# Performance work log

Hardware: AMD Instinct MI355X
Metric: run time of the kernel (lower is better)

The kernel has to match this reference:

```python
import jax, jax.numpy as jnp
import numpy as np

V_TGT, V_CMP = 100, 100
E_ENC, E_DEC = 5, 128
H_ENC, H_DEC = 256, 512
B, S, T = 128, 120, 120
GO = 0


def _p(key, shape, scale=0.08):
    return scale * jax.random.normal(key, shape, dtype=jnp.float32)


def setup_inputs() -> dict:
    key = jax.random.key(0)
    ks = iter(jax.random.split(key, 48))
    inp = {}
    inp['tgts'] = jax.random.randint(next(ks), (B, S), 0, V_TGT)
    inp['cmps'] = jax.random.randint(next(ks), (B, T), 0, V_CMP)
    inp['emb_enc'] = _p(next(ks), (V_TGT, E_ENC))
    for d in ('f', 'b'):
        inp['enc_Wih_' + d] = _p(next(ks), (3 * H_ENC, E_ENC))
        inp['enc_Whh_' + d] = _p(next(ks), (3 * H_ENC, H_ENC))
        inp['enc_bih_' + d] = jnp.zeros((3 * H_ENC,), jnp.float32)
        inp['enc_bhh_' + d] = jnp.zeros((3 * H_ENC,), jnp.float32)
    inp['emb_dec'] = _p(next(ks), (V_CMP, E_DEC))
    inp['attn_W'] = _p(next(ks), (H_DEC, 2 * H_DEC))
    inp['attn_b'] = jnp.zeros((H_DEC,), jnp.float32)
    inp['attn_v'] = _p(next(ks), (H_DEC,))
    dims = [E_DEC + H_DEC, H_DEC, H_DEC]
    for l in range(3):
        inp['dec_Wih%d' % l] = _p(next(ks), (3 * H_DEC, dims[l]))
        inp['dec_Whh%d' % l] = _p(next(ks), (3 * H_DEC, H_DEC))
        inp['dec_bih%d' % l] = jnp.zeros((3 * H_DEC,), jnp.float32)
        inp['dec_bhh%d' % l] = jnp.zeros((3 * H_DEC,), jnp.float32)
    inp['out_W'] = _p(next(ks), (V_CMP, H_DEC))
    inp['out_b'] = jnp.zeros((V_CMP,), jnp.float32)
    return inp


def gru_cell(x, h, Wih, Whh, bih, bhh):
    gi = x @ Wih.T + bih
    gh = h @ Whh.T + bhh
    ir, iz, inn = jnp.split(gi, 3, axis=-1)
    hr, hz, hn = jnp.split(gh, 3, axis=-1)
    r = jax.nn.sigmoid(ir + hr)
    z = jax.nn.sigmoid(iz + hz)
    n = jnp.tanh(inn + r * hn)
    return (1.0 - z) * n + z * h


def run_gru(xs, h0, Wih, Whh, bih, bhh, reverse=False):
    # xs: (S, B, in); returns outputs (S, B, H) and final hidden (B, H)
    def step(h, x):
        h2 = gru_cell(x, h, Wih, Whh, bih, bhh)
        return h2, h2
    hT, outs = jax.lax.scan(step, h0, xs, reverse=reverse)
    return outs, hT


def _forward(tgts, cmps, emb_enc, enc_Wih_f, enc_Whh_f, enc_bih_f, enc_bhh_f,
             enc_Wih_b, enc_Whh_b, enc_bih_b, enc_bhh_b, emb_dec,
             attn_W, attn_b, attn_v,
             dec_Wih0, dec_Whh0, dec_bih0, dec_bhh0,
             dec_Wih1, dec_Whh1, dec_bih1, dec_bhh1,
             dec_Wih2, dec_Whh2, dec_bih2, dec_bhh2,
             out_W, out_b):
    b = tgts.shape[0]
    # ---- encoder: bidirectional GRU ----
    xs = emb_enc[tgts].transpose(1, 0, 2)  # (S, B, E_ENC)
    h0 = jnp.zeros((b, H_ENC), jnp.float32)
    out_f, h_f = run_gru(xs, h0, enc_Wih_f, enc_Whh_f, enc_bih_f, enc_bhh_f)
    out_b_, h_b = run_gru(xs, h0, enc_Wih_b, enc_Whh_b, enc_bih_b, enc_bhh_b, reverse=True)
    enc_out = jnp.concatenate([out_f, out_b_], -1).transpose(1, 0, 2)  # (B, S, 512)
    h_enc = jnp.concatenate([h_f, h_b], -1)                             # (B, 512)
    hidden = jnp.zeros((3, b, H_DEC), jnp.float32).at[0].set(h_enc)
    # ---- decoder: teacher-forced inputs [GO, cmps[:, :-1]] ----
    x_seq = jnp.concatenate([jnp.full((b, 1), GO, cmps.dtype), cmps[:, :-1]], 1).T  # (T, B)

    def dec_step(h, x_t):
        emb = emb_dec[x_t]                                   # (B, 128)
        hq = h[0]                                            # (B, 512)
        cat = jnp.concatenate(
            [jnp.broadcast_to(hq[:, None, :], enc_out.shape), enc_out], -1)  # (B, S, 1024)
        energy = jnp.tanh(cat @ attn_W.T + attn_b)           # (B, S, 512)
        score = energy @ attn_v                              # (B, S)
        attn = jax.nn.softmax(score, axis=-1)
        ctx = jnp.einsum('bs,bsh->bh', attn, enc_out)        # (B, 512)
        inp = jnp.concatenate([emb, ctx], -1)                # (B, 640)
        h0n = gru_cell(inp, h[0], dec_Wih0, dec_Whh0, dec_bih0, dec_bhh0)
        h1n = gru_cell(h0n, h[1], dec_Wih1, dec_Whh1, dec_bih1, dec_bhh1)
        h2n = gru_cell(h1n, h[2], dec_Wih2, dec_Whh2, dec_bih2, dec_bhh2)
        logit = h2n @ out_W.T + out_b                        # (B, V_CMP)
        return jnp.stack([h0n, h1n, h2n]), jax.nn.log_softmax(logit, axis=-1)

    _, scores = jax.lax.scan(jax.checkpoint(dec_step), hidden, x_seq)
    return scores.transpose(1, 0, 2)  # (B, T, V_CMP)


def reference(tgts, cmps, emb_enc, enc_Wih_f, enc_Whh_f, enc_bih_f, enc_bhh_f,
              enc_Wih_b, enc_Whh_b, enc_bih_b, enc_bhh_b, emb_dec,
              attn_W, attn_b, attn_v,
              dec_Wih0, dec_Whh0, dec_bih0, dec_bhh0,
              dec_Wih1, dec_Whh1, dec_bih1, dec_bhh1,
              dec_Wih2, dec_Whh2, dec_bih2, dec_bhh2,
              out_W, out_b):
    return _forward(tgts, cmps, emb_enc, enc_Wih_f, enc_Whh_f, enc_bih_f, enc_bhh_f,
                    enc_Wih_b, enc_Whh_b, enc_bih_b, enc_bhh_b, emb_dec,
                    attn_W, attn_b, attn_v,
                    dec_Wih0, dec_Whh0, dec_bih0, dec_bhh0,
                    dec_Wih1, dec_Whh1, dec_bih1, dec_bhh1,
                    dec_Wih2, dec_Whh2, dec_bih2, dec_bhh2,
                    out_W, out_b)
```

## Files before the change

### kernel.cpp

```cpp
#include <hip/hip_runtime.h>
#include <math.h>

#define B_   128
#define S_   120
#define T_   120
#define HENC 256
#define HDEC 512
#define VCMP 100

#define OFF_EMBGI_F   0
#define OFF_EMBGI_B   76800
#define OFF_EMBGI_D   153600
#define OFF_HENC      307200
#define OFF_HDEC      438272
#define OFF_HQP       831488
#define OFF_CTX       1093632
#define OFF_GIP       1159168
#define OFF_GHP       1945600
#define OFF_ENCOUT    2732032
#define OFF_ENCATT    10596352
#define WS_FLOATS     18460672

#define PSTRIDE_D 196608
#define PSTRIDE_Q 65536

__device__ __forceinline__ float sigm(float x)      { return 1.0f / (1.0f + __expf(-x)); }
__device__ __forceinline__ float tanh_fast(float x) { return 1.0f - 2.0f / (1.0f + __expf(2.0f * x)); }

__device__ __forceinline__ float wred_sum(float v) {
#pragma unroll
  for (int m = 32; m > 0; m >>= 1) v += __shfl_xor(v, m);
  return v;
}
__device__ __forceinline__ float wred_max(float v) {
#pragma unroll
  for (int m = 32; m > 0; m >>= 1) v = fmaxf(v, __shfl_xor(v, m));
  return v;
}

__global__ void k_zero(float* p, int n) {
  int i = blockIdx.x * blockDim.x + threadIdx.x;
  if (i < n) p[i] = 0.0f;
}

__global__ void k_embgi_enc(const float* emb, const float* Wf, const float* bf,
                            const float* Wb, const float* bb, float* outf, float* outb) {
  int idx = blockIdx.x * blockDim.x + threadIdx.x;
  const float* W  = blockIdx.y ? Wb : Wf;
  const float* bi = blockIdx.y ? bb : bf;
  float* o        = blockIdx.y ? outb : outf;
  int v = idx / 768, j = idx % 768;
  float a = bi[j];
#pragma unroll
  for (int e = 0; e < 5; e++) a = fmaf(emb[v * 5 + e], W[j * 5 + e], a);
  o[idx] = a;
}

__global__ void k_embgi_dec(const float* emb, const float* Wih0, const float* bih0, float* out) {
  int idx = blockIdx.x * blockDim.x + threadIdx.x;
  int v = idx / 1536, j = idx % 1536;
  float a = bih0[j];
  const float4* er = (const float4*)(emb + v * 128);
  const float4* wr = (const float4*)(Wih0 + (size_t)j * 640);
#pragma unroll 8
  for (int e = 0; e < 32; e++) {
    float4 ev = er[e], wv = wr[e];
    a = fmaf(ev.x, wv.x, a); a = fmaf(ev.y, wv.y, a);
    a = fmaf(ev.z, wv.z, a); a = fmaf(ev.w, wv.w, a);
  }
  out[idx] = a;
}

struct GemmJob {
  const float* A; const float* W; float* C; const float* bias;
  int lda, ldw, N;
};

__global__ __launch_bounds__(256) void k_gemm64(GemmJob ja, GemmJob jb, int splits, int Kc, int Cstride) {
  GemmJob jj = ((int)blockIdx.z < splits) ? ja : jb;
  int sp = blockIdx.z % splits;
  int k0 = sp * Kc;
  float* C = jj.C + (size_t)sp * Cstride;
  int tid = threadIdx.x;
  int tx = tid & 15, ty = tid >> 4;
  int m0 = blockIdx.y * 64, n0 = blockIdx.x * 64;
  __shared__ float As[16][68];
  __shared__ float Ws[16][68];
  float acc[4][4] = {};
  int r = tid >> 2, c = tid & 3;
  const float* Ap = jj.A + (size_t)(m0 + r) * jj.lda + k0 + c * 4;
  const float* Wp = jj.W + (size_t)(n0 + r) * jj.ldw + k0 + c * 4;
  for (int kt = 0; kt < Kc; kt += 16) {
    float4 av = *(const float4*)(Ap + kt);
    float4 wv = *(const float4*)(Wp + kt);
    __syncthreads();
    As[c * 4 + 0][r] = av.x; As[c * 4 + 1][r] = av.y; As[c * 4 + 2][r] = av.z; As[c * 4 + 3][r] = av.w;
    Ws[c * 4 + 0][r] = wv.x; Ws[c * 4 + 1][r] = wv.y; Ws[c * 4 + 2][r] = wv.z; Ws[c * 4 + 3][r] = wv.w;
    __syncthreads();
#pragma unroll
    for (int kk = 0; kk < 16; kk++) {
      float4 a = *(const float4*)&As[kk][ty * 4];
      float4 w = *(const float4*)&Ws[kk][tx * 4];
      float am[4] = {a.x, a.y, a.z, a.w}, wn[4] = {w.x, w.y, w.z, w.w};
#pragma unroll
      for (int i = 0; i < 4; i++)
#pragma unroll
        for (int j2 = 0; j2 < 4; j2++) acc[i][j2] = fmaf(am[i], wn[j2], acc[i][j2]);
    }
  }
  int N = jj.N;
  float bv[4] = {0, 0, 0, 0};
  if (jj.bias) {
#pragma unroll
    for (int j2 = 0; j2 < 4; j2++) bv[j2] = jj.bias[n0 + tx * 4 + j2];
  }
#pragma unroll
  for (int i = 0; i < 4; i++) {
    float4 v = {acc[i][0] + bv[0], acc[i][1] + bv[1], acc[i][2] + bv[2], acc[i][3] + bv[3]};
    *(float4*)(C + (size_t)(m0 + ty * 4 + i) * N + n0 + tx * 4) = v;
  }
}

__global__ __launch_bounds__(256) void k_gemm128(GemmJob ja, GemmJob jb, int splits, int Kc, int Cstride) {
  GemmJob jj = ((int)blockIdx.z < splits) ? ja : jb;
  int sp = blockIdx.z % splits;
  int k0 = sp * Kc;
  float* C = jj.C + (size_t)sp * Cstride;
  int tid = threadIdx.x;
  int tx = tid & 15, ty = tid >> 4;
  int m0 = blockIdx.y * 128, n0 = blockIdx.x * 128;
  __shared__ float As[16][132];
  __shared__ float Ws[16][132];
  float acc[8][8] = {};
  for (int kt = 0; kt < Kc; kt += 16) {
    float4 av[2], wv[2];
#pragma unroll
    for (int h = 0; h < 2; h++) {
      int idx = tid + h * 256;
      int r = idx >> 2, c = idx & 3;
      av[h] = *(const float4*)(jj.A + (size_t)(m0 + r) * jj.lda + k0 + kt + c * 4);
      wv[h] = *(const float4*)(jj.W + (size_t)(n0 + r) * jj.ldw + k0 + kt + c * 4);
    }
    __syncthreads();
#pragma unroll
    for (int h = 0; h < 2; h++) {
      int idx = tid + h * 256;
      int r = idx >> 2, c = idx & 3;
      As[c * 4 + 0][r] = av[h].x; As[c * 4 + 1][r] = av[h].y; As[c * 4 + 2][r] = av[h].z; As[c * 4 + 3][r] = av[h].w;
      Ws[c * 4 + 0][r] = wv[h].x; Ws[c * 4 + 1][r] = wv[h].y; Ws[c * 4 + 2][r] = wv[h].z; Ws[c * 4 + 3][r] = wv[h].w;
    }
    __syncthreads();
#pragma unroll
    for (int kk = 0; kk < 16; kk++) {
      float4 a0 = *(const float4*)&As[kk][ty * 4];
      float4 a1 = *(const float4*)&As[kk][ty * 4 + 64];
      float4 w0 = *(const float4*)&Ws[kk][tx * 4];
      float4 w1 = *(const float4*)&Ws[kk][tx * 4 + 64];
      float am[8] = {a0.x, a0.y, a0.z, a0.w, a1.x, a1.y, a1.z, a1.w};
      float wn[8] = {w0.x, w0.y, w0.z, w0.w, w1.x, w1.y, w1.z, w1.w};
#pragma unroll
      for (int i = 0; i < 8; i++)
#pragma unroll
        for (int j2 = 0; j2 < 8; j2++) acc[i][j2] = fmaf(am[i], wn[j2], acc[i][j2]);
    }
  }
  int N = jj.N;
  float bv[8] = {0, 0, 0, 0, 0, 0, 0, 0};
  if (jj.bias) {
#pragma unroll
    for (int j2 = 0; j2 < 4; j2++) {
      bv[j2]     = jj.bias[n0 + tx * 4 + j2];
      bv[4 + j2] = jj.bias[n0 + 64 + tx * 4 + j2];
    }
  }
#pragma unroll
  for (int i = 0; i < 8; i++) {
    int m = m0 + ((i < 4) ? (ty * 4 + i) : (64 + ty * 4 + (i - 4)));
    float4 v0 = {acc[i][0] + bv[0], acc[i][1] + bv[1], acc[i][2] + bv[2], acc[i][3] + bv[3]};
    float4 v1 = {acc[i][4] + bv[4], acc[i][5] + bv[5], acc[i][6] + bv[6], acc[i][7] + bv[7]};
    *(float4*)(C + (size_t)m * N + n0 + tx * 4) = v0;
    *(float4*)(C + (size_t)m * N + n0 + 64 + tx * 4) = v1;
  }
}

__global__ void k_gate_enc(const float* ghP, const float* tabf, const float* tabb,
                           const float* bhhf, const float* bhhb, const int* tgts,
                           const float* hfc, float* hfn, const float* hbc, float* hbn,
                           float* enc_out, int t) {
  int g = blockIdx.x * blockDim.x + threadIdx.x;
  int d = g >> 15, rem = g & 32767, b = rem >> 8, j = rem & 255;
  int sidx = d ? (S_ - 1 - t) : t;
  int tok = tgts[b * S_ + sidx];
  const float* gh  = ghP + (size_t)(d * 2) * PSTRIDE_D + b * 768;
  const float* bh  = d ? bhhb : bhhf;
  const float* tab = (d ? tabb : tabf) + (size_t)tok * 768;
  float hr  = gh[j]       + gh[PSTRIDE_D + j]       + bh[j];
  float hz  = gh[j + 256] + gh[PSTRIDE_D + j + 256] + bh[j + 256];
  float hnn = gh[j + 512] + gh[PSTRIDE_D + j + 512] + bh[j + 512];
  float rr = sigm(tab[j] + hr);
  float zz = sigm(tab[j + 256] + hz);
  float nn = tanh_fast(tab[j + 512] + rr * hnn);
  const float* hc = d ? hbc : hfc;
  float*       hx = d ? hbn : hfn;
  float h0 = hc[b * 256 + j];
  float h2 = (1.0f - zz) * nn + zz * h0;
  hx[b * 256 + j] = h2;
  enc_out[((size_t)b * S_ + sidx) * 512 + d * 256 + j] = h2;
}

__global__ void k_h0init(const float* hf, const float* hb, float* h0) {
  int g = blockIdx.x * blockDim.x + threadIdx.x;
  int b = g >> 9, j = g & 511;
  h0[g] = (j < 256) ? hf[b * 256 + j] : hb[b * 256 + (j - 256)];
}

__global__ __launch_bounds__(256) void k_att_ctx(const float* hqP, const float* enc_att,
                                                 const float* enc_out, const float* av,
                                                 float* ctx) {
  int b = blockIdx.x;
  __shared__ float hq[512];
  __shared__ float vs[512];
  __shared__ float sc[128];
  __shared__ float red[8];
  int tid = threadIdx.x, w = tid >> 6, lane = tid & 63;
  for (int d = tid; d < 512; d += 256) {
    hq[d] = hqP[b * 512 + d] + hqP[PSTRIDE_Q + b * 512 + d] +
            hqP[2 * PSTRIDE_Q + b * 512 + d] + hqP[3 * PSTRIDE_Q + b * 512 + d];
    vs[d] = av[d];
  }
  __syncthreads();
  for (int i = 0; i < 30; i++) {
    int s = w + 4 * i;
    const float4* ea = (const float4*)(enc_att + ((size_t)b * S_ + s) * 512) + lane * 2;
    float4 e0 = ea[0], e1 = ea[1];
    int d0 = lane * 8;
    float a;
    a  = vs[d0 + 0] * tanh_fast(e0.x + hq[d0 + 0]);
    a += vs[d0 + 1] * tanh_fast(e0.y + hq[d0 + 1]);
    a += vs[d0 + 2] * tanh_fast(e0.z + hq[d0 + 2]);
    a += vs[d0 + 3] * tanh_fast(e0.w + hq[d0 + 3]);
    a += vs[d0 + 4] * tanh_fast(e1.x + hq[d0 + 4]);
    a += vs[d0 + 5] * tanh_fast(e1.y + hq[d0 + 5]);
    a += vs[d0 + 6] * tanh_fast(e1.z + hq[d0 + 6]);
    a += vs[d0 + 7] * tanh_fast(e1.w + hq[d0 + 7]);
    a = wred_sum(a);
    if (lane == 0) sc[s] = a;
  }
  __syncthreads();
  float x = (tid < S_) ? sc[tid] : -1e30f;
  float mx = wred_max(x);
  if (lane == 0) red[w] = mx;
  __syncthreads();
  mx = fmaxf(fmaxf(red[0], red[1]), fmaxf(red[2], red[3]));
  float e = (tid < S_) ? __expf(x - mx) : 0.0f;
  float sm = wred_sum(e);
  if (lane == 0) red[4 + w] = sm;
  __syncthreads();
  float inv = 1.0f / (red[4] + red[5] + red[6] + red[7]);
  if (tid < S_) sc[tid] = e * inv;
  __syncthreads();
  for (int h = tid; h < 512; h += 256) {
    float cacc = 0.0f;
    const float* eo = enc_out + (size_t)b * S_ * 512 + h;
#pragma unroll 4
    for (int s = 0; s < S_; s++) cacc = fmaf(sc[s], eo[(size_t)s * 512], cacc);
    ctx[b * 512 + h] = cacc;
  }
}

__global__ void k_gate_dec(const float* giP, const float* ghP, const float* gtab,
                           const int* cmps, int t, const float* bih, const float* bhh,
                           const float* hp, float* hn) {
  int g = blockIdx.x * blockDim.x + threadIdx.x;
  int b = g >> 9, j = g & 511;
  int base = b * 1536 + j;
  float gr  = giP[base]        + giP[PSTRIDE_D + base]        + giP[2 * PSTRIDE_D + base]        + giP[3 * PSTRIDE_D + base];
  float gz  = giP[base + 512]  + giP[PSTRIDE_D + base + 512]  + giP[2 * PSTRIDE_D + base + 512]  + giP[3 * PSTRIDE_D + base + 512];
  float gn  = giP[base + 1024] + giP[PSTRIDE_D + base + 1024] + giP[2 * PSTRIDE_D + base + 1024] + giP[3 * PSTRIDE_D + base + 1024];
  float hr  = ghP[base]        + ghP[PSTRIDE_D + base]        + ghP[2 * PSTRIDE_D + base]        + ghP[3 * PSTRIDE_D + base]        + bhh[j];
  float hz  = ghP[base + 512]  + ghP[PSTRIDE_D + base + 512]  + ghP[2 * PSTRIDE_D + base + 512]  + ghP[3 * PSTRIDE_D + base + 512]  + bhh[j + 512];
  float hnn = ghP[base + 1024] + ghP[PSTRIDE_D + base + 1024] + ghP[2 * PSTRIDE_D + base + 1024] + ghP[3 * PSTRIDE_D + base + 1024] + bhh[j + 1024];
  float er, ez, en;
  if (gtab) {
    int tok = (t == 0) ? 0 : cmps[b * T_ + (t - 1)];
    const float* row = gtab + (size_t)tok * 1536;
    er = row[j]; ez = row[j + 512]; en = row[j + 1024];
  } else {
    er = bih[j]; ez = bih[j + 512]; en = bih[j + 1024];
  }
  float rr = sigm(gr + er + hr);
  float zz = sigm(gz + ez + hz);
  float nn = tanh_fast(gn + en + rr * hnn);
  float h0 = hp[b * 512 + j];
  hn[b * 512 + j] = (1.0f - zz) * nn + zz * h0;
}

__global__ __launch_bounds__(256) void k_out(const float* h2, const float* oW, const float* ob,
                                             float* out, int t) {
  int b = blockIdx.x;
  __shared__ float hs[512];
  __shared__ float lg[104];
  __shared__ float red[8];
  int tid = threadIdx.x, w = tid >> 6, lane = tid & 63;
  for (int d = tid; d < 512; d += 256) hs[d] = h2[b * 512 + d];
  __syncthreads();
  for (int i = 0; i < 25; i++) {
    int n = w + 4 * i;
    const float4* wr = (const float4*)(oW + (size_t)n * 512) + lane * 2;
    float4 w0 = wr[0], w1 = wr[1];
    const float* hp = &hs[lane * 8];
    float a = w0.x * hp[0] + w0.y * hp[1] + w0.z * hp[2] + w0.w * hp[3] +
              w1.x * hp[4] + w1.y * hp[5] + w1.z * hp[6] + w1.w * hp[7];
    a = wred_sum(a);
    if (lane == 0) lg[n] = a + ob[n];
  }
  __syncthreads();
  float x = (tid < VCMP) ? lg[tid] : -1e30f;
  float mx = wred_max(x);
  if (lane == 0) red[w] = mx;
  __syncthreads();
  mx = fmaxf(fmaxf(red[0], red[1]), fmaxf(red[2], red[3]));
  float e = (tid < VCMP) ? __expf(x - mx) : 0.0f;
  float sm = wred_sum(e);
  if (lane == 0) red[4 + w] = sm;
  __syncthreads();
  float lse = mx + logf(red[4] + red[5] + red[6] + red[7]);
  if (tid < VCMP) out[((size_t)b * T_ + t) * VCMP + tid] = x - lse;
}

extern "C" void kernel_launch(void* const* d_in, const int* in_sizes, int n_in,
                              void* d_out, int out_size, void* d_ws, size_t ws_size,
                              hipStream_t stream) {
  (void)in_sizes; (void)n_in; (void)out_size; (void)ws_size;
  const int*   tgts    = (const int*)d_in[0];
  const int*   cmps    = (const int*)d_in[1];
  const float* emb_enc = (const float*)d_in[2];
  const float* eWih_f  = (const float*)d_in[3];
  const float* eWhh_f  = (const float*)d_in[4];
  const float* ebih_f  = (const float*)d_in[5];
  const float* ebhh_f  = (const float*)d_in[6];
  const float* eWih_b  = (const float*)d_in[7];
  const float* eWhh_b  = (const float*)d_in[8];
  const float* ebih_b  = (const float*)d_in[9];
  const float* ebhh_b  = (const float*)d_in[10];
  const float* emb_dec = (const float*)d_in[11];
  const float* attn_W  = (const float*)d_in[12];
  const float* attn_b  = (const float*)d_in[13];
  const float* attn_v  = (const float*)d_in[14];
  const float* dWih0   = (const float*)d_in[15];
  const float* dWhh0   = (const float*)d_in[16];
  const float* dbih0   = (const float*)d_in[17];  (void)dbih0;
  const float* dbhh0   = (const float*)d_in[18];
  const float* dWih1   = (const float*)d_in[19];
  const float* dWhh1   = (const float*)d_in[20];
  const float* dbih1   = (const float*)d_in[21];
  const float* dbhh1   = (const float*)d_in[22];
  const float* dWih2   = (const float*)d_in[23];
  const float* dWhh2   = (const float*)d_in[24];
  const float* dbih2   = (const float*)d_in[25];
  const float* dbhh2   = (const float*)d_in[26];
  const float* out_W   = (const float*)d_in[27];
  const float* out_b   = (const float*)d_in[28];
  float* out = (float*)d_out;
  float* ws  = (float*)d_ws;

  float* emb_gi_f = ws + OFF_EMBGI_F;
  float* emb_gi_b = ws + OFF_EMBGI_B;
  float* emb_gi_d = ws + OFF_EMBGI_D;
  float* h_enc    = ws + OFF_HENC;
  float* h_dec    = ws + OFF_HDEC;
  float* hqP      = ws + OFF_HQP;
  float* ctx      = ws + OFF_CTX;
  float* giP      = ws + OFF_GIP;
  float* ghP      = ws + OFF_GHP;
  float* enc_out  = ws + OFF_ENCOUT;
  float* enc_att  = ws + OFF_ENCATT;

  k_embgi_enc<<<dim3(300, 2), 256, 0, stream>>>(emb_enc, eWih_f, ebih_f, eWih_b, ebih_b, emb_gi_f, emb_gi_b);
  k_embgi_dec<<<600, 256, 0, stream>>>(emb_dec, dWih0, dbih0, emb_gi_d);
  {
    int nz = 2 * 2 * B_ * HENC + 2 * 3 * B_ * HDEC;
    k_zero<<<(nz + 255) / 256, 256, 0, stream>>>(h_enc, nz);
  }

  for (int t = 0; t < S_; t++) {
    int cur = t & 1, nxt = cur ^ 1;
    GemmJob ja = {h_enc + 0 * 65536 + cur * 32768, eWhh_f, giP, nullptr, 256, 256, 768};
    GemmJob jb = {h_enc + 1 * 65536 + cur * 32768, eWhh_b, giP + 2 * PSTRIDE_D, nullptr, 256, 256, 768};
    k_gemm64<<<dim3(12, 2, 4), 256, 0, stream>>>(ja, jb, 2, 128, PSTRIDE_D);
    k_gate_enc<<<256, 256, 0, stream>>>(giP, emb_gi_f, emb_gi_b, ebhh_f, ebhh_b, tgts,
                                        h_enc + cur * 32768, h_enc + nxt * 32768,
                                        h_enc + 65536 + cur * 32768, h_enc + 65536 + nxt * 32768,
                                        enc_out, t);
  }
  k_h0init<<<256, 256, 0, stream>>>(h_enc, h_enc + 65536, h_dec);

  {
    GemmJob ja = {enc_out, attn_W + 512, enc_att, attn_b, 512, 1024, 512};
    k_gemm128<<<dim3(4, 120, 1), 256, 0, stream>>>(ja, ja, 1, 512, 0);
  }

  for (int t = 0; t < T_; t++) {
    int cur = t & 1, nxt = cur ^ 1;
    float* h0c = h_dec + cur * 196608;
    float* h1c = h0c + 65536;
    float* h2c = h0c + 131072;
    float* h0n = h_dec + nxt * 196608;
    float* h1n = h0n + 65536;
    float* h2n = h0n + 131072;
    (void)h2c;

    GemmJob jq = {h0c, attn_W, hqP, nullptr, 512, 1024, 512};
    k_gemm64<<<dim3(8, 2, 4), 256, 0, stream>>>(jq, jq, 4, 128, PSTRIDE_Q);
    k_att_ctx<<<128, 256, 0, stream>>>(hqP, enc_att, enc_out, attn_v, ctx);

    GemmJob g0a = {ctx, dWih0 + 128, giP, nullptr, 512, 640, 1536};
    GemmJob g0b = {h0c, dWhh0, ghP, nullptr, 512, 512, 1536};
    k_gemm128<<<dim3(12, 1, 8), 256, 0, stream>>>(g0a, g0b, 4, 128, PSTRIDE_D);
    k_gate_dec<<<256, 256, 0, stream>>>(giP, ghP, emb_gi_d, cmps, t, nullptr, dbhh0, h0c, h0n);

    GemmJob g1a = {h0n, dWih1, giP, nullptr, 512, 512, 1536};
    GemmJob g1b = {h1c, dWhh1, ghP, nullptr, 512, 512, 1536};
    k_gemm128<<<dim3(12, 1, 8), 256, 0, stream>>>(g1a, g1b, 4, 128, PSTRIDE_D);
    k_gate_dec<<<256, 256, 0, stream>>>(giP, ghP, nullptr, nullptr, t, dbih1, dbhh1, h1c, h1n);

    GemmJob g2a = {h1n, dWih2, giP, nullptr, 512, 512, 1536};
    GemmJob g2b = {h2c, dWhh2, ghP, nullptr, 512, 512, 1536};
    k_gemm128<<<dim3(12, 1, 8), 256, 0, stream>>>(g2a, g2b, 4, 128, PSTRIDE_D);
    k_gate_dec<<<256, 256, 0, stream>>>(giP, ghP, nullptr, nullptr, t, dbih2, dbhh2, h2c, h2n);

    k_out<<<128, 256, 0, stream>>>(h2n, out_W, out_b, out, t);
  }
}
```

Before: 17.35 ms.

## Rewrite encoder/decoder recurrences with fp16 MFMA fused GEMM+gate kernels

Replaces the fp32 SIMT GEMMs with fp16 MFMA 16x16x32 kernels and fuses each GRU step's hidden GEMM with its gate nonlinearity. All recurrent-weight matmuls that depend only on the previous step's hidden states (attention query plus the three decoder Whh) are batched into one concatenated-weight GEMM per step. The output projection and log-softmax are moved out of the time loop into one batched GEMM over all steps. Weights, encoder outputs and attention keys are converted to fp16 up front, cutting launch count and memory traffic, at the cost of reduced precision in the recurrent path.

```diff
diff --git a/kernel.cpp b/kernel.cpp
--- a/kernel.cpp
+++ b/kernel.cpp
@@ -4,25 +4,36 @@
 #define B_   128
 #define S_   120
 #define T_   120
-#define HENC 256
-#define HDEC 512
 #define VCMP 100
 
-#define OFF_EMBGI_F   0
-#define OFF_EMBGI_B   76800
-#define OFF_EMBGI_D   153600
-#define OFF_HENC      307200
-#define OFF_HDEC      438272
-#define OFF_HQP       831488
-#define OFF_CTX       1093632
-#define OFF_GIP       1159168
-#define OFF_GHP       1945600
-#define OFF_ENCOUT    2732032
-#define OFF_ENCATT    10596352
-#define WS_FLOATS     18460672
-
-#define PSTRIDE_D 196608
-#define PSTRIDE_Q 65536
+typedef _Float16 f16;
+typedef _Float16 f16x8 __attribute__((ext_vector_type(8)));
+typedef float f32x4 __attribute__((ext_vector_type(4)));
+
+#define MFMA16(a,b,c) __builtin_amdgcn_mfma_f32_16x16x32_f16(a, b, c, 0, 0, 0)
+
+#define OFF_TAB_F    0
+#define OFF_TAB_B    76800
+#define OFF_TAB_D    153600
+#define OFF_HENC32   307200
+#define OFF_HENC16   438272
+#define OFF_HDEC32   503808
+#define OFF_HDEC16   897024
+#define OFF_CA       1028096
+#define OFF_CTX32    1683456
+#define OFF_CTX16    1748992
+#define OFF_H2ALL    1781760
+#define OFF_ENCOUT   5746688
+#define OFF_ENCATT   9678848
+#define OFF_LOGITS   13611008
+#define OFF_WCAT     15577088
+#define OFF_WIH0C    16887808
+#define OFF_WIH1     17281024
+#define OFF_WIH2     17674240
+#define OFF_UE       18067456
+#define OFF_EWHH     18198528
+#define OFF_OW       18395136
+#define WS_FLOATS    18427904
 
 __device__ __forceinline__ float sigm(float x)      { return 1.0f / (1.0f + __expf(-x)); }
 __device__ __forceinline__ float tanh_fast(float x) { return 1.0f - 2.0f / (1.0f + __expf(2.0f * x)); }
@@ -41,6 +52,13 @@
 __global__ void k_zero(float* p, int n) {
   int i = blockIdx.x * blockDim.x + threadIdx.x;
   if (i < n) p[i] = 0.0f;
+}
+
+__global__ void k_cvt(const float* src, f16* dst, int rows, int cols, int ldsrc, int off) {
+  int i = blockIdx.x * blockDim.x + threadIdx.x;
+  if (i >= rows * cols) return;
+  int r = i / cols, c = i - r * cols;
+  dst[(size_t)r * cols + c] = (f16)src[(size_t)r * ldsrc + off + c];
 }
 
 __global__ void k_embgi_enc(const float* emb, const float* Wf, const float* bf,
@@ -71,152 +89,166 @@
   out[idx] = a;
 }
 
-struct GemmJob {
-  const float* A; const float* W; float* C; const float* bias;
-  int lda, ldw, N;
-};
-
-__global__ __launch_bounds__(256) void k_gemm64(GemmJob ja, GemmJob jb, int splits, int Kc, int Cstride) {
-  GemmJob jj = ((int)blockIdx.z < splits) ? ja : jb;
-  int sp = blockIdx.z % splits;
-  int k0 = sp * Kc;
-  float* C = jj.C + (size_t)sp * Cstride;
-  int tid = threadIdx.x;
-  int tx = tid & 15, ty = tid >> 4;
-  int m0 = blockIdx.y * 64, n0 = blockIdx.x * 64;
-  __shared__ float As[16][68];
-  __shared__ float Ws[16][68];
-  float acc[4][4] = {};
-  int r = tid >> 2, c = tid & 3;
-  const float* Ap = jj.A + (size_t)(m0 + r) * jj.lda + k0 + c * 4;
-  const float* Wp = jj.W + (size_t)(n0 + r) * jj.ldw + k0 + c * 4;
-  for (int kt = 0; kt < Kc; kt += 16) {
-    float4 av = *(const float4*)(Ap + kt);
-    float4 wv = *(const float4*)(Wp + kt);
-    __syncthreads();
-    As[c * 4 + 0][r] = av.x; As[c * 4 + 1][r] = av.y; As[c * 4 + 2][r] = av.z; As[c * 4 + 3][r] = av.w;
-    Ws[c * 4 + 0][r] = wv.x; Ws[c * 4 + 1][r] = wv.y; Ws[c * 4 + 2][r] = wv.z; Ws[c * 4 + 3][r] = wv.w;
-    __syncthreads();
-#pragma unroll
-    for (int kk = 0; kk < 16; kk++) {
-      float4 a = *(const float4*)&As[kk][ty * 4];
-      float4 w = *(const float4*)&Ws[kk][tx * 4];
-      float am[4] = {a.x, a.y, a.z, a.w}, wn[4] = {w.x, w.y, w.z, w.w};
-#pragma unroll
-      for (int i = 0; i < 4; i++)
-#pragma unroll
-        for (int j2 = 0; j2 < 4; j2++) acc[i][j2] = fmaf(am[i], wn[j2], acc[i][j2]);
-    }
-  }
-  int N = jj.N;
-  float bv[4] = {0, 0, 0, 0};
-  if (jj.bias) {
-#pragma unroll
-    for (int j2 = 0; j2 < 4; j2++) bv[j2] = jj.bias[n0 + tx * 4 + j2];
-  }
-#pragma unroll
-  for (int i = 0; i < 4; i++) {
-    float4 v = {acc[i][0] + bv[0], acc[i][1] + bv[1], acc[i][2] + bv[2], acc[i][3] + bv[3]};
-    *(float4*)(C + (size_t)(m0 + ty * 4 + i) * N + n0 + tx * 4) = v;
-  }
-}
-
-__global__ __launch_bounds__(256) void k_gemm128(GemmJob ja, GemmJob jb, int splits, int Kc, int Cstride) {
-  GemmJob jj = ((int)blockIdx.z < splits) ? ja : jb;
-  int sp = blockIdx.z % splits;
-  int k0 = sp * Kc;
-  float* C = jj.C + (size_t)sp * Cstride;
-  int tid = threadIdx.x;
-  int tx = tid & 15, ty = tid >> 4;
-  int m0 = blockIdx.y * 128, n0 = blockIdx.x * 128;
-  __shared__ float As[16][132];
-  __shared__ float Ws[16][132];
-  float acc[8][8] = {};
-  for (int kt = 0; kt < Kc; kt += 16) {
-    float4 av[2], wv[2];
-#pragma unroll
-    for (int h = 0; h < 2; h++) {
-      int idx = tid + h * 256;
-      int r = idx >> 2, c = idx & 3;
-      av[h] = *(const float4*)(jj.A + (size_t)(m0 + r) * jj.lda + k0 + kt + c * 4);
-      wv[h] = *(const float4*)(jj.W + (size_t)(n0 + r) * jj.ldw + k0 + kt + c * 4);
-    }
-    __syncthreads();
-#pragma unroll
-    for (int h = 0; h < 2; h++) {
-      int idx = tid + h * 256;
-      int r = idx >> 2, c = idx & 3;
-      As[c * 4 + 0][r] = av[h].x; As[c * 4 + 1][r] = av[h].y; As[c * 4 + 2][r] = av[h].z; As[c * 4 + 3][r] = av[h].w;
-      Ws[c * 4 + 0][r] = wv[h].x; Ws[c * 4 + 1][r] = wv[h].y; Ws[c * 4 + 2][r] = wv[h].z; Ws[c * 4 + 3][r] = wv[h].w;
-    }
-    __syncthreads();
-#pragma unroll
-    for (int kk = 0; kk < 16; kk++) {
-      float4 a0 = *(const float4*)&As[kk][ty * 4];
-      float4 a1 = *(const float4*)&As[kk][ty * 4 + 64];
-      float4 w0 = *(const float4*)&Ws[kk][tx * 4];
-      float4 w1 = *(const float4*)&Ws[kk][tx * 4 + 64];
-      float am[8] = {a0.x, a0.y, a0.z, a0.w, a1.x, a1.y, a1.z, a1.w};
-      float wn[8] = {w0.x, w0.y, w0.z, w0.w, w1.x, w1.y, w1.z, w1.w};
-#pragma unroll
-      for (int i = 0; i < 8; i++)
-#pragma unroll
-        for (int j2 = 0; j2 < 8; j2++) acc[i][j2] = fmaf(am[i], wn[j2], acc[i][j2]);
-    }
-  }
-  int N = jj.N;
-  float bv[8] = {0, 0, 0, 0, 0, 0, 0, 0};
-  if (jj.bias) {
-#pragma unroll
-    for (int j2 = 0; j2 < 4; j2++) {
-      bv[j2]     = jj.bias[n0 + tx * 4 + j2];
-      bv[4 + j2] = jj.bias[n0 + 64 + tx * 4 + j2];
-    }
-  }
-#pragma unroll
-  for (int i = 0; i < 8; i++) {
-    int m = m0 + ((i < 4) ? (ty * 4 + i) : (64 + ty * 4 + (i - 4)));
-    float4 v0 = {acc[i][0] + bv[0], acc[i][1] + bv[1], acc[i][2] + bv[2], acc[i][3] + bv[3]};
-    float4 v1 = {acc[i][4] + bv[4], acc[i][5] + bv[5], acc[i][6] + bv[6], acc[i][7] + bv[7]};
-    *(float4*)(C + (size_t)m * N + n0 + tx * 4) = v0;
-    *(float4*)(C + (size_t)m * N + n0 + 64 + tx * 4) = v1;
-  }
-}
-
-__global__ void k_gate_enc(const float* ghP, const float* tabf, const float* tabb,
-                           const float* bhhf, const float* bhhb, const int* tgts,
-                           const float* hfc, float* hfn, const float* hbc, float* hbn,
-                           float* enc_out, int t) {
-  int g = blockIdx.x * blockDim.x + threadIdx.x;
-  int d = g >> 15, rem = g & 32767, b = rem >> 8, j = rem & 255;
-  int sidx = d ? (S_ - 1 - t) : t;
-  int tok = tgts[b * S_ + sidx];
-  const float* gh  = ghP + (size_t)(d * 2) * PSTRIDE_D + b * 768;
-  const float* bh  = d ? bhhb : bhhf;
-  const float* tab = (d ? tabb : tabf) + (size_t)tok * 768;
-  float hr  = gh[j]       + gh[PSTRIDE_D + j]       + bh[j];
-  float hz  = gh[j + 256] + gh[PSTRIDE_D + j + 256] + bh[j + 256];
-  float hnn = gh[j + 512] + gh[PSTRIDE_D + j + 512] + bh[j + 512];
-  float rr = sigm(tab[j] + hr);
-  float zz = sigm(tab[j + 256] + hz);
-  float nn = tanh_fast(tab[j + 512] + rr * hnn);
-  const float* hc = d ? hbc : hfc;
-  float*       hx = d ? hbn : hfn;
-  float h0 = hc[b * 256 + j];
-  float h2 = (1.0f - zz) * nn + zz * h0;
-  hx[b * 256 + j] = h2;
-  enc_out[((size_t)b * S_ + sidx) * 512 + d * 256 + j] = h2;
-}
-
-__global__ void k_h0init(const float* hf, const float* hb, float* h0) {
+__global__ void k_h0init(const float* hf, const float* hb, float* h32, f16* h16) {
   int g = blockIdx.x * blockDim.x + threadIdx.x;
   int b = g >> 9, j = g & 511;
-  h0[g] = (j < 256) ? hf[b * 256 + j] : hb[b * 256 + (j - 256)];
-}
-
-__global__ __launch_bounds__(256) void k_att_ctx(const float* hqP, const float* enc_att,
-                                                 const float* enc_out, const float* av,
-                                                 float* ctx) {
+  float v = (j < 256) ? hf[b * 256 + j] : hb[b * 256 + (j - 256)];
+  h32[g] = v; h16[g] = (f16)v;
+}
+
+template<int NC>
+__device__ __forceinline__ void gemm_core(const f16* A, int ldA, const f16* W, int ldW,
+                                          int chunkRows, int K, int m0, int n0,
+                                          int lane, int wm, int wn, f32x4 acc[2][2][NC]) {
+  const f16* Ap0 = A + (size_t)(m0 + wm * 32 + (lane & 15)) * ldA + ((lane >> 4) << 3);
+  const f16* Ap1 = Ap0 + (size_t)16 * ldA;
+  const f16* Wp0 = W + (size_t)(n0 + wn * 32 + (lane & 15)) * ldW + ((lane >> 4) << 3);
+  const f16* Wp1 = Wp0 + (size_t)16 * ldW;
+#pragma unroll 2
+  for (int k = 0; k < K; k += 32) {
+    f16x8 a0 = *(const f16x8*)(Ap0 + k);
+    f16x8 a1 = *(const f16x8*)(Ap1 + k);
+#pragma unroll
+    for (int c = 0; c < NC; c++) {
+      const f16* w0 = Wp0 + (size_t)c * chunkRows * ldW + k;
+      const f16* w1 = Wp1 + (size_t)c * chunkRows * ldW + k;
+      f16x8 b0 = *(const f16x8*)w0;
+      f16x8 b1 = *(const f16x8*)w1;
+      acc[0][0][c] = MFMA16(a0, b0, acc[0][0][c]);
+      acc[1][0][c] = MFMA16(a1, b0, acc[1][0][c]);
+      acc[0][1][c] = MFMA16(a0, b1, acc[0][1][c]);
+      acc[1][1][c] = MFMA16(a1, b1, acc[1][1][c]);
+    }
+  }
+}
+
+__global__ __launch_bounds__(256) void k_phaseA(const f16* h0, const f16* h1, const f16* h2,
+                                                const f16* Wcat, float* CA) {
+  int n0 = blockIdx.x * 64, m0 = blockIdx.y * 64;
+  int tid = threadIdx.x, lane = tid & 63, w = tid >> 6, wm = w >> 1, wn = w & 1;
+  const f16* A = (n0 < 2048) ? h0 : (n0 < 3584 ? h1 : h2);
+  f32x4 acc[2][2][1] = {};
+  gemm_core<1>(A, 512, Wcat, 512, 0, 512, m0, n0, lane, wm, wn, acc);
+#pragma unroll
+  for (int i = 0; i < 2; i++)
+#pragma unroll
+    for (int j = 0; j < 2; j++) {
+      int mb = m0 + wm * 32 + i * 16 + ((lane >> 4) << 2);
+      int n  = n0 + wn * 32 + j * 16 + (lane & 15);
+#pragma unroll
+      for (int r = 0; r < 4; r++) CA[(size_t)(mb + r) * 5120 + n] = acc[i][j][0][r];
+    }
+}
+
+template<bool OUT16>
+__global__ __launch_bounds__(256) void k_gemm_bias(const f16* A, int ldA, const f16* W, int ldW,
+                                                   const float* bias, int nbias, void* Cout,
+                                                   int ldC, int K) {
+  int n0 = blockIdx.x * 64, m0 = blockIdx.y * 64;
+  int tid = threadIdx.x, lane = tid & 63, w = tid >> 6, wm = w >> 1, wn = w & 1;
+  f32x4 acc[2][2][1] = {};
+  gemm_core<1>(A, ldA, W, ldW, 0, K, m0, n0, lane, wm, wn, acc);
+#pragma unroll
+  for (int i = 0; i < 2; i++)
+#pragma unroll
+    for (int j = 0; j < 2; j++) {
+      int mb = m0 + wm * 32 + i * 16 + ((lane >> 4) << 2);
+      int n  = n0 + wn * 32 + j * 16 + (lane & 15);
+      float bv = (bias && n < nbias) ? bias[n] : 0.0f;
+#pragma unroll
+      for (int r = 0; r < 4; r++) {
+        float v = acc[i][j][0][r] + bv;
+        if (OUT16) ((f16*)Cout)[(size_t)(mb + r) * ldC + n] = (f16)v;
+        else       ((float*)Cout)[(size_t)(mb + r) * ldC + n] = v;
+      }
+    }
+}
+
+__global__ __launch_bounds__(256) void k_dec_layer(const f16* Ah, const f16* W3, const float* CA,
+                                                   int ghoff, const float* tab, const int* cmps,
+                                                   int t, const float* bih, const float* bhh,
+                                                   const float* hprev, float* hout32, f16* hout16) {
+  int n0 = blockIdx.x * 64, m0 = blockIdx.y * 64;
+  int tid = threadIdx.x, lane = tid & 63, w = tid >> 6, wm = w >> 1, wn = w & 1;
+  f32x4 acc[2][2][3] = {};
+  gemm_core<3>(Ah, 512, W3, 512, 512, 512, m0, n0, lane, wm, wn, acc);
+#pragma unroll
+  for (int i = 0; i < 2; i++)
+#pragma unroll
+    for (int j = 0; j < 2; j++) {
+      int mb = m0 + wm * 32 + i * 16 + ((lane >> 4) << 2);
+      int n  = n0 + wn * 32 + j * 16 + (lane & 15);
+#pragma unroll
+      for (int r = 0; r < 4; r++) {
+        int m = mb + r;
+        const float* ghp = CA + (size_t)m * 5120 + ghoff + n;
+        float hr  = ghp[0]    + bhh[n];
+        float hz  = ghp[512]  + bhh[n + 512];
+        float hnn = ghp[1024] + bhh[n + 1024];
+        float er, ez, en;
+        if (tab) {
+          int tok = t ? cmps[m * T_ + (t - 1)] : 0;
+          const float* row = tab + (size_t)tok * 1536;
+          er = row[n]; ez = row[n + 512]; en = row[n + 1024];
+        } else {
+          er = bih[n]; ez = bih[n + 512]; en = bih[n + 1024];
+        }
+        float rr = sigm(acc[i][j][0][r] + er + hr);
+        float zz = sigm(acc[i][j][1][r] + ez + hz);
+        float nn = tanh_fast(acc[i][j][2][r] + en + rr * hnn);
+        float hv = (1.0f - zz) * nn + zz * hprev[(size_t)m * 512 + n];
+        hout32[(size_t)m * 512 + n] = hv;
+        hout16[(size_t)m * 512 + n] = (f16)hv;
+      }
+    }
+}
+
+__global__ __launch_bounds__(256) void k_enc_step(const f16* h16base, const f16* Whh,
+                                                  const float* tabf, const float* tabb,
+                                                  const float* bhhf, const float* bhhb,
+                                                  const int* tgts, const float* h32base,
+                                                  float* h32out, f16* h16out, f16* enc_out,
+                                                  int t, int cur) {
+  int n0 = blockIdx.x * 64, m0 = blockIdx.y * 64, dir = blockIdx.z;
+  int tid = threadIdx.x, lane = tid & 63, w = tid >> 6, wm = w >> 1, wn = w & 1;
+  const f16* A = h16base + dir * 65536 + cur * 32768;
+  const f16* W = Whh + (size_t)dir * 768 * 256;
+  f32x4 acc[2][2][3] = {};
+  gemm_core<3>(A, 256, W, 256, 256, 256, m0, n0, lane, wm, wn, acc);
+  int sidx = dir ? (S_ - 1 - t) : t;
+  const float* bh  = dir ? bhhb : bhhf;
+  const float* tb  = dir ? tabb : tabf;
+  const float* h32 = h32base + dir * 65536 + cur * 32768;
+  float* ho32      = h32out + dir * 65536;
+  f16*   ho16      = h16out + dir * 65536;
+#pragma unroll
+  for (int i = 0; i < 2; i++)
+#pragma unroll
+    for (int j = 0; j < 2; j++) {
+      int mb = m0 + wm * 32 + i * 16 + ((lane >> 4) << 2);
+      int n  = n0 + wn * 32 + j * 16 + (lane & 15);
+#pragma unroll
+      for (int r = 0; r < 4; r++) {
+        int b = mb + r;
+        int tok = tgts[b * S_ + sidx];
+        const float* row = tb + (size_t)tok * 768;
+        float hr  = acc[i][j][0][r] + bh[n];
+        float hz  = acc[i][j][1][r] + bh[n + 256];
+        float hnn = acc[i][j][2][r] + bh[n + 512];
+        float rr = sigm(row[n] + hr);
+        float zz = sigm(row[n + 256] + hz);
+        float nn = tanh_fast(row[n + 512] + rr * hnn);
+        float hv = (1.0f - zz) * nn + zz * h32[b * 256 + n];
+        ho32[b * 256 + n] = hv;
+        ho16[b * 256 + n] = (f16)hv;
+        enc_out[((size_t)b * S_ + sidx) * 512 + dir * 256 + n] = (f16)hv;
+      }
+    }
+}
+
+__global__ __launch_bounds__(256) void k_att(const float* CA, const f16* enc_att,
+                                             const f16* enc_out, const float* av,
+                                             float* ctx32, f16* ctx16) {
   int b = blockIdx.x;
   __shared__ float hq[512];
   __shared__ float vs[512];
@@ -224,25 +256,17 @@
   __shared__ float red[8];
   int tid = threadIdx.x, w = tid >> 6, lane = tid & 63;
   for (int d = tid; d < 512; d += 256) {
-    hq[d] = hqP[b * 512 + d] + hqP[PSTRIDE_Q + b * 512 + d] +
-            hqP[2 * PSTRIDE_Q + b * 512 + d] + hqP[3 * PSTRIDE_Q + b * 512 + d];
+    hq[d] = CA[(size_t)b * 5120 + d];
     vs[d] = av[d];
   }
   __syncthreads();
   for (int i = 0; i < 30; i++) {
     int s = w + 4 * i;
-    const float4* ea = (const float4*)(enc_att + ((size_t)b * S_ + s) * 512) + lane * 2;
-    float4 e0 = ea[0], e1 = ea[1];
+    f16x8 e = ((const f16x8*)(enc_att + ((size_t)b * S_ + s) * 512))[lane];
     int d0 = lane * 8;
-    float a;
-    a  = vs[d0 + 0] * tanh_fast(e0.x + hq[d0 + 0]);
-    a += vs[d0 + 1] * tanh_fast(e0.y + hq[d0 + 1]);
-    a += vs[d0 + 2] * tanh_fast(e0.z + hq[d0 + 2]);
-    a += vs[d0 + 3] * tanh_fast(e0.w + hq[d0 + 3]);
-    a += vs[d0 + 4] * tanh_fast(e1.x + hq[d0 + 4]);
-    a += vs[d0 + 5] * tanh_fast(e1.y + hq[d0 + 5]);
-    a += vs[d0 + 6] * tanh_fast(e1.z + hq[d0 + 6]);
-    a += vs[d0 + 7] * tanh_fast(e1.w + hq[d0 + 7]);
+    float a = 0.0f;
+#pragma unroll
+    for (int q = 0; q < 8; q++) a += vs[d0 + q] * tanh_fast((float)e[q] + hq[d0 + q]);
     a = wred_sum(a);
     if (lane == 0) sc[s] = a;
   }
@@ -261,71 +285,29 @@
   __syncthreads();
   for (int h = tid; h < 512; h += 256) {
     float cacc = 0.0f;
-    const float* eo = enc_out + (size_t)b * S_ * 512 + h;
+    const f16* eo = enc_out + (size_t)b * S_ * 512 + h;
 #pragma unroll 4
-    for (int s = 0; s < S_; s++) cacc = fmaf(sc[s], eo[(size_t)s * 512], cacc);
-    ctx[b * 512 + h] = cacc;
-  }
-}
-
-__global__ void k_gate_dec(const float* giP, const float* ghP, const float* gtab,
-                           const int* cmps, int t, const float* bih, const float* bhh,
-                           const float* hp, float* hn) {
-  int g = blockIdx.x * blockDim.x + threadIdx.x;
-  int b = g >> 9, j = g & 511;
-  int base = b * 1536 + j;
-  float gr  = giP[base]        + giP[PSTRIDE_D + base]        + giP[2 * PSTRIDE_D + base]        + giP[3 * PSTRIDE_D + base];
-  float gz  = giP[base + 512]  + giP[PSTRIDE_D + base + 512]  + giP[2 * PSTRIDE_D + base + 512]  + giP[3 * PSTRIDE_D + base + 512];
-  float gn  = giP[base + 1024] + giP[PSTRIDE_D + base + 1024] + giP[2 * PSTRIDE_D + base + 1024] + giP[3 * PSTRIDE_D + base + 1024];
-  float hr  = ghP[base]        + ghP[PSTRIDE_D + base]        + ghP[2 * PSTRIDE_D + base]        + ghP[3 * PSTRIDE_D + base]        + bhh[j];
-  float hz  = ghP[base + 512]  + ghP[PSTRIDE_D + base + 512]  + ghP[2 * PSTRIDE_D + base + 512]  + ghP[3 * PSTRIDE_D + base + 512]  + bhh[j + 512];
-  float hnn = ghP[base + 1024] + ghP[PSTRIDE_D + base + 1024] + ghP[2 * PSTRIDE_D + base + 1024] + ghP[3 * PSTRIDE_D + base + 1024] + bhh[j + 1024];
-  float er, ez, en;
-  if (gtab) {
-    int tok = (t == 0) ? 0 : cmps[b * T_ + (t - 1)];
-    const float* row = gtab + (size_t)tok * 1536;
-    er = row[j]; ez = row[j + 512]; en = row[j + 1024];
-  } else {
-    er = bih[j]; ez = bih[j + 512]; en = bih[j + 1024];
-  }
-  float rr = sigm(gr + er + hr);
-  float zz = sigm(gz + ez + hz);
-  float nn = tanh_fast(gn + en + rr * hnn);
-  float h0 = hp[b * 512 + j];
-  hn[b * 512 + j] = (1.0f - zz) * nn + zz * h0;
-}
-
-__global__ __launch_bounds__(256) void k_out(const float* h2, const float* oW, const float* ob,
-                                             float* out, int t) {
-  int b = blockIdx.x;
-  __shared__ float hs[512];
-  __shared__ float lg[104];
-  __shared__ float red[8];
-  int tid = threadIdx.x, w = tid >> 6, lane = tid & 63;
-  for (int d = tid; d < 512; d += 256) hs[d] = h2[b * 512 + d];
-  __syncthreads();
-  for (int i = 0; i < 25; i++) {
-    int n = w + 4 * i;
-    const float4* wr = (const float4*)(oW + (size_t)n * 512) + lane * 2;
-    float4 w0 = wr[0], w1 = wr[1];
-    const float* hp = &hs[lane * 8];
-    float a = w0.x * hp[0] + w0.y * hp[1] + w0.z * hp[2] + w0.w * hp[3] +
-              w1.x * hp[4] + w1.y * hp[5] + w1.z * hp[6] + w1.w * hp[7];
-    a = wred_sum(a);
-    if (lane == 0) lg[n] = a + ob[n];
-  }
-  __syncthreads();
-  float x = (tid < VCMP) ? lg[tid] : -1e30f;
-  float mx = wred_max(x);
-  if (lane == 0) red[w] = mx;
-  __syncthreads();
-  mx = fmaxf(fmaxf(red[0], red[1]), fmaxf(red[2], red[3]));
-  float e = (tid < VCMP) ? __expf(x - mx) : 0.0f;
+    for (int s = 0; s < S_; s++) cacc = fmaf(sc[s], (float)eo[(size_t)s * 512], cacc);
+    ctx32[b * 512 + h] = cacc;
+    ctx16[b * 512 + h] = (f16)cacc;
+  }
+}
+
+__global__ __launch_bounds__(256) void k_lsm(const float* lg, float* out) {
+  int row = blockIdx.x * 4 + (threadIdx.x >> 6);
+  int lane = threadIdx.x & 63;
+  const float* L = lg + (size_t)row * 128;
+  float x1 = (lane < VCMP) ? L[lane] : -1e30f;
+  float x2 = (lane + 64 < VCMP) ? L[lane + 64] : -1e30f;
+  float mx = wred_max(fmaxf(x1, x2));
+  float e = ((lane < VCMP) ? __expf(x1 - mx) : 0.0f) +
+            ((lane + 64 < VCMP) ? __expf(x2 - mx) : 0.0f);
   float sm = wred_sum(e);
-  if (lane == 0) red[4 + w] = sm;
-  __syncthreads();
-  float lse = mx + logf(red[4] + red[5] + red[6] + red[7]);
-  if (tid < VCMP) out[((size_t)b * T_ + t) * VCMP + tid] = x - lse;
+  float lse = mx + logf(sm);
+  int t = row >> 7, b = row & 127;
+  float* o = out + ((size_t)b * T_ + t) * VCMP;
+  if (lane < VCMP) o[lane] = x1 - lse;
+  if (lane + 64 < VCMP) o[lane + 64] = x2 - lse;
 }
 
 extern "C" void kernel_launch(void* const* d_in, const int* in_sizes, int n_in,
@@ -349,7 +331,7 @@
   const float* attn_v  = (const float*)d_in[14];
   const float* dWih0   = (const float*)d_in[15];
   const float* dWhh0   = (const float*)d_in[16];
-  const float* dbih0   = (const float*)d_in[17];  (void)dbih0;
+  const float* dbih0   = (const float*)d_in[17];
   const float* dbhh0   = (const float*)d_in[18];
   const float* dWih1   = (const float*)d_in[19];
   const float* dWhh1   = (const float*)d_in[20];
@@ -364,71 +346,81 @@
   float* out = (float*)d_out;
   float* ws  = (float*)d_ws;
 
-  float* emb_gi_f = ws + OFF_EMBGI_F;
-  float* emb_gi_b = ws + OFF_EMBGI_B;
-  float* emb_gi_d = ws + OFF_EMBGI_D;
-  float* h_enc    = ws + OFF_HENC;
-  float* h_dec    = ws + OFF_HDEC;
-  float* hqP      = ws + OFF_HQP;
-  float* ctx      = ws + OFF_CTX;
-  float* giP      = ws + OFF_GIP;
-  float* ghP      = ws + OFF_GHP;
-  float* enc_out  = ws + OFF_ENCOUT;
-  float* enc_att  = ws + OFF_ENCATT;
-
-  k_embgi_enc<<<dim3(300, 2), 256, 0, stream>>>(emb_enc, eWih_f, ebih_f, eWih_b, ebih_b, emb_gi_f, emb_gi_b);
-  k_embgi_dec<<<600, 256, 0, stream>>>(emb_dec, dWih0, dbih0, emb_gi_d);
-  {
-    int nz = 2 * 2 * B_ * HENC + 2 * 3 * B_ * HDEC;
-    k_zero<<<(nz + 255) / 256, 256, 0, stream>>>(h_enc, nz);
-  }
+  float* tabF     = ws + OFF_TAB_F;
+  float* tabB     = ws + OFF_TAB_B;
+  float* tabD     = ws + OFF_TAB_D;
+  float* henc32   = ws + OFF_HENC32;
+  f16*   henc16   = (f16*)(ws + OFF_HENC16);
+  float* hdec32   = ws + OFF_HDEC32;
+  f16*   hdec16   = (f16*)(ws + OFF_HDEC16);
+  float* CA       = ws + OFF_CA;
+  float* ctx32    = ws + OFF_CTX32;
+  f16*   ctx16    = (f16*)(ws + OFF_CTX16);
+  f16*   H2all    = (f16*)(ws + OFF_H2ALL);
+  f16*   encout16 = (f16*)(ws + OFF_ENCOUT);
+  f16*   encatt16 = (f16*)(ws + OFF_ENCATT);
+  float* logits   = ws + OFF_LOGITS;
+  f16*   Wcat     = (f16*)(ws + OFF_WCAT);
+  f16*   Wih0c    = (f16*)(ws + OFF_WIH0C);
+  f16*   Wih1h    = (f16*)(ws + OFF_WIH1);
+  f16*   Wih2h    = (f16*)(ws + OFF_WIH2);
+  f16*   Ueh      = (f16*)(ws + OFF_UE);
+  f16*   eWhhh    = (f16*)(ws + OFF_EWHH);
+  f16*   oWh      = (f16*)(ws + OFF_OW);
+
+  k_zero<<<(720896 + 255) / 256, 256, 0, stream>>>(ws + OFF_HENC32, 720896);
+  k_zero<<<(32768 + 255) / 256, 256, 0, stream>>>(ws + OFF_H2ALL, 32768);
+  k_zero<<<(32768 + 255) / 256, 256, 0, stream>>>(ws + OFF_OW, 32768);
+  k_embgi_enc<<<dim3(300, 2), 256, 0, stream>>>(emb_enc, eWih_f, ebih_f, eWih_b, ebih_b, tabF, tabB);
+  k_embgi_dec<<<600, 256, 0, stream>>>(emb_dec, dWih0, dbih0, tabD);
+  auto cvt = [&](const float* src, f16* dst, int rows, int cols, int ldsrc, int off) {
+    int n = rows * cols;
+    k_cvt<<<(n + 255) / 256, 256, 0, stream>>>(src, dst, rows, cols, ldsrc, off);
+  };
+  cvt(attn_W, Wcat,               512, 512, 1024, 0);
+  cvt(dWhh0,  Wcat + 512 * 512,  1536, 512, 512, 0);
+  cvt(dWhh1,  Wcat + 2048 * 512, 1536, 512, 512, 0);
+  cvt(dWhh2,  Wcat + 3584 * 512, 1536, 512, 512, 0);
+  cvt(dWih0,  Wih0c,             1536, 512, 640, 128);
+  cvt(dWih1,  Wih1h,             1536, 512, 512, 0);
+  cvt(dWih2,  Wih2h,             1536, 512, 512, 0);
+  cvt(attn_W, Ueh,                512, 512, 1024, 512);
+  cvt(eWhh_f, eWhhh,              768, 256, 256, 0);
+  cvt(eWhh_b, eWhhh + 768 * 256,  768, 256, 256, 0);
+  cvt(out_W,  oWh,                100, 512, 512, 0);
 
   for (int t = 0; t < S_; t++) {
     int cur = t & 1, nxt = cur ^ 1;
-    GemmJob ja = {h_enc + 0 * 65536 + cur * 32768, eWhh_f, giP, nullptr, 256, 256, 768};
-    GemmJob jb = {h_enc + 1 * 65536 + cur * 32768, eWhh_b, giP + 2 * PSTRIDE_D, nullptr, 256, 256, 768};
-    k_gemm64<<<dim3(12, 2, 4), 256, 0, stream>>>(ja, jb, 2, 128, PSTRIDE_D);
-    k_gate_enc<<<256, 256, 0, stream>>>(giP, emb_gi_f, emb_gi_b, ebhh_f, ebhh_b, tgts,
-                                        h_enc + cur * 32768, h_enc + nxt * 32768,
-                                        h_enc + 65536 + cur * 32768, h_enc + 65536 + nxt * 32768,
-                                        enc_out, t);
-  }
-  k_h0init<<<256, 256, 0, stream>>>(h_enc, h_enc + 65536, h_dec);
-
-  {
-    GemmJob ja = {enc_out, attn_W + 512, enc_att, attn_b, 512, 1024, 512};
-    k_gemm128<<<dim3(4, 120, 1), 256, 0, stream>>>(ja, ja, 1, 512, 0);
-  }
+    k_enc_step<<<dim3(4, 2, 2), 256, 0, stream>>>(
+        henc16, eWhhh, tabF, tabB, ebhh_f, ebhh_b, tgts, henc32,
+        henc32 + nxt * 32768, henc16 + nxt * 32768, encout16, t, cur);
+  }
+  k_h0init<<<256, 256, 0, stream>>>(henc32, henc32 + 65536, hdec32, hdec16);
+
+  k_gemm_bias<true><<<dim3(8, 240), 256, 0, stream>>>(encout16, 512, Ueh, 512, attn_b, 512,
+                                                      encatt16, 512, 512);
 
   for (int t = 0; t < T_; t++) {
     int cur = t & 1, nxt = cur ^ 1;
-    float* h0c = h_dec + cur * 196608;
-    float* h1c = h0c + 65536;
-    float* h2c = h0c + 131072;
-    float* h0n = h_dec + nxt * 196608;
-    float* h1n = h0n + 65536;
-    float* h2n = h0n + 131072;
-    (void)h2c;
-
-    GemmJob jq = {h0c, attn_W, hqP, nullptr, 512, 1024, 512};
-    k_gemm64<<<dim3(8, 2, 4), 256, 0, stream>>>(jq, jq, 4, 128, PSTRIDE_Q);
-    k_att_ctx<<<128, 256, 0, stream>>>(hqP, enc_att, enc_out, attn_v, ctx);
-
-    GemmJob g0a = {ctx, dWih0 + 128, giP, nullptr, 512, 640, 1536};
-    GemmJob g0b = {h0c, dWhh0, ghP, nullptr, 512, 512, 1536};
-    k_gemm128<<<dim3(12, 1, 8), 256, 0, stream>>>(g0a, g0b, 4, 128, PSTRIDE_D);
-    k_gate_dec<<<256, 256, 0, stream>>>(giP, ghP, emb_gi_d, cmps, t, nullptr, dbhh0, h0c, h0n);
-
-    GemmJob g1a = {h0n, dWih1, giP, nullptr, 512, 512, 1536};
-    GemmJob g1b = {h1c, dWhh1, ghP, nullptr, 512, 512, 1536};
-    k_gemm128<<<dim3(12, 1, 8), 256, 0, stream>>>(g1a, g1b, 4, 128, PSTRIDE_D);
-    k_gate_dec<<<256, 256, 0, stream>>>(giP, ghP, nullptr, nullptr, t, dbih1, dbhh1, h1c, h1n);
-
-    GemmJob g2a = {h1n, dWih2, giP, nullptr, 512, 512, 1536};
-    GemmJob g2b = {h2c, dWhh2, ghP, nullptr, 512, 512, 1536};
-    k_gemm128<<<dim3(12, 1, 8), 256, 0, stream>>>(g2a, g2b, 4, 128, PSTRIDE_D);
-    k_gate_dec<<<256, 256, 0, stream>>>(giP, ghP, nullptr, nullptr, t, dbih2, dbhh2, h2c, h2n);
-
-    k_out<<<128, 256, 0, stream>>>(h2n, out_W, out_b, out, t);
-  }
-}
+    const f16* h0c16 = hdec16 + cur * 131072;
+    const f16* h1c16 = hdec16 + cur * 131072 + 65536;
+    const f16* h2c16 = H2all + (size_t)t * 65536;
+    k_phaseA<<<dim3(80, 2), 256, 0, stream>>>(h0c16, h1c16, h2c16, Wcat, CA);
+    k_att<<<128, 256, 0, stream>>>(CA, encatt16, encout16, attn_v, ctx32, ctx16);
+    k_dec_layer<<<dim3(8, 2), 256, 0, stream>>>(
+        ctx16, Wih0c, CA, 512, tabD, cmps, t, nullptr, dbhh0,
+        hdec32 + cur * 196608, hdec32 + nxt * 196608, hdec16 + nxt * 131072);
+    k_dec_layer<<<dim3(8, 2), 256, 0, stream>>>(
+        hdec16 + nxt * 131072, Wih1h, CA, 2048, nullptr, nullptr, t, dbih1, dbhh1,
+        hdec32 + cur * 196608 + 65536, hdec32 + nxt * 196608 + 65536,
+        hdec16 + nxt * 131072 + 65536);
+    k_dec_layer<<<dim3(8, 2), 256, 0, stream>>>(
+        hdec16 + nxt * 131072 + 65536, Wih2h, CA, 3584, nullptr, nullptr, t, dbih2, dbhh2,
+        hdec32 + cur * 196608 + 131072, hdec32 + nxt * 196608 + 131072,
+        H2all + (size_t)(t + 1) * 65536);
+  }
+
+  k_gemm_bias<false><<<dim3(2, 240), 256, 0, stream>>>(H2all + 65536, 512, oWh, 512, out_b, VCMP,
+                                                       logits, 128, 512);
+  k_lsm<<<3840, 256, 0, stream>>>(logits, out);
+}
```

Result: faster. 16.87 ms (-2.8%).
